# Kernel tuning notes

Measured on AMD Instinct MI355X. Metric: run time of the kernel, lower is better.

Reference implementation:

```python
import jax, jax.numpy as jnp
import numpy as np

EPS = 1e-7


def setup_inputs() -> dict:
    key = jax.random.key(0)
    k1, k2, k3 = jax.random.split(key, 3)
    B, IN, OUT = 256, 256, 512
    x = jax.random.uniform(k1, (B, IN), dtype=jnp.float32)
    w = jax.random.uniform(k2, (IN, OUT), dtype=jnp.float32)
    t = jax.random.uniform(k3, (B, OUT), dtype=jnp.float32)
    return {"x": x, "w": w, "t": t}


def reference(x, w, t):
    # x: [B, IN], w: [IN, OUT], t: [B, OUT]
    xe = x[:, :, None]          # [B, IN, 1]
    te = t[:, None, :]          # [B, 1, OUT]
    we = w[None, :, :]          # [1, IN, OUT]

    one = jnp.asarray(1.0, dtype=x.dtype)
    # rel_x: relevance of x, reduced over batch dim 0 -> [1, IN, OUT]
    rel_x = jnp.minimum(te / (xe + EPS), one).sum(axis=0, keepdims=True) \
            / xe.sum(axis=0, keepdims=True)
    # rel_w: relevance of w, reduced over IN dim -> [B, 1, OUT]
    rel_w = jnp.minimum(te / (we + EPS), one).sum(axis=-2, keepdims=True) \
            / xe.sum(axis=-2, keepdims=True)

    ind_x = jnp.argmax(xe * rel_x, axis=-2, keepdims=True)  # [B, 1, OUT]
    ind_w = jnp.argmax(rel_w * we, axis=-2, keepdims=True)  # [B, 1, OUT]

    inner_x = xe * jax.lax.stop_gradient(we)  # [B, IN, OUT]
    inner_w = jax.lax.stop_gradient(xe) * we  # [B, IN, OUT]

    chosen_x = jnp.take_along_axis(inner_x, ind_x, axis=-2).squeeze(-2)  # [B, OUT]
    chosen_w = jnp.take_along_axis(inner_w, ind_w, axis=-2).squeeze(-2)  # [B, OUT]
    return chosen_x, chosen_w
```

## Files before the change

kernel.cpp:

```cpp
#include <hip/hip_runtime.h>

constexpr int B   = 256;
constexpr int IN  = 256;
constexpr int OUT = 512;
constexpr double EPSD = 1e-7;

typedef unsigned long long ull;


__global__ __launch_bounds__(256) void k_setup(const float* __restrict__ x,
        double* __restrict__ rxd, double* __restrict__ part, float* __restrict__ xt) {
    const int tid = threadIdx.x;
    const int blk = blockIdx.x;
    if (blk < 32) {
        const int b0 = blk * 8;
        #pragma unroll
        for (int k = 0; k < 8; ++k)
            rxd[(b0 + k) * IN + tid] = 1.0 / ((double)x[(b0 + k) * IN + tid] + EPSD);
    } else if (blk < 40) {
        const int j = blk - 32, b0 = j * 32;
        double s0 = 0, s1 = 0, s2 = 0, s3 = 0;
        #pragma unroll
        for (int k = 0; k < 32; k += 4) {
            s0 += (double)x[(b0 + k + 0) * IN + tid];
            s1 += (double)x[(b0 + k + 1) * IN + tid];
            s2 += (double)x[(b0 + k + 2) * IN + tid];
            s3 += (double)x[(b0 + k + 3) * IN + tid];
        }
        part[j * IN + tid] = (s0 + s1) + (s2 + s3);
    } else {
        const int i0 = (blk - 40) * 32;
        for (int k = 0; k < 32; ++k)
            xt[(i0 + k) * B + tid] = x[tid * IN + (i0 + k)];
    }
}

__global__ __launch_bounds__(512, 2) void k_main(const float* __restrict__ w,
        const float* __restrict__ t, const double* __restrict__ rxd,
        const double* __restrict__ part, const float* __restrict__ xt,
        float* __restrict__ out) {
    const int tid  = threadIdx.x;
    const int half = tid >> 8;
    const int j    = tid & 255;
    const int o    = blockIdx.x * 2 + half;

    __shared__ double tc[2][B];
    __shared__ double rp[2][2][IN];
    __shared__ double rc[2][IN];
    __shared__ ull    keys[2][2][B];
    __shared__ ull    swv[8];

    {
        float wv = w[j * OUT + o];
        ull key = ((ull)__float_as_uint(wv) << 8) | (unsigned)(255 - j);
        #pragma unroll
        for (int off = 32; off; off >>= 1) {
            ull v = __shfl_down(key, off);
            key = v > key ? v : key;
        }
        if ((tid & 63) == 0) swv[tid >> 6] = key;
    }

    tc[half][j] = (double)t[j * OUT + o];
    double ps = 0.0;
    #pragma unroll
    for (int k = 0; k < 8; ++k) ps += part[k * IN + j];
    const double rcolv = 1.0 / ps;
    __syncthreads();

    ull wk = swv[half * 4];
    #pragma unroll
    for (int k = 1; k < 4; ++k) { ull v = swv[half * 4 + k]; wk = v > wk ? v : wk; }
    const int warg_o = 255 - (int)(wk & 0xFFull);

    {
        const int i0 = (j & 127) * 2;
        const int bh = j >> 7;
        const double* __restrict__ tcc  = tc[half] + bh * 128;
        const double* __restrict__ base = rxd + (size_t)(bh * 128) * IN + i0;
        double a0 = 0, a1 = 0, a2 = 0, a3 = 0;
        #pragma unroll 8
        for (int k = 0; k < 128; k += 2) {
            double2 r0 = *(const double2*)(base + (size_t)k * IN);
            double2 r1 = *(const double2*)(base + (size_t)(k + 1) * IN);
            double t0 = tcc[k], t1 = tcc[k + 1];
            a0 += fmin(t0 * r0.x, 1.0);
            a1 += fmin(t0 * r0.y, 1.0);
            a2 += fmin(t1 * r1.x, 1.0);
            a3 += fmin(t1 * r1.y, 1.0);
        }
        rp[half][bh][i0]     = a0 + a2;
        rp[half][bh][i0 + 1] = a1 + a3;
    }
    __syncthreads();
    rc[half][j] = (rp[half][0][j] + rp[half][1][j]) * rcolv;
    __syncthreads();

    {
        const int b0 = (j & 127) * 2;
        const int ih = j >> 7;
        const double* __restrict__ rcc = rc[half];
        double mA0 = -1.0, mA1 = -1.0, mB0 = -1.0, mB1 = -1.0;
        #pragma unroll 8
        for (int i = ih * 128; i < ih * 128 + 128; i += 2) {
            float2 x0 = *(const float2*)&xt[(size_t)i * B + b0];
            float2 x1 = *(const float2*)&xt[(size_t)(i + 1) * B + b0];
            double s00 = (double)x0.x * rcc[i];
            double s01 = (double)x0.y * rcc[i];
            double s10 = (double)x1.x * rcc[i + 1];
            double s11 = (double)x1.y * rcc[i + 1];
            long long u00 = (__double_as_longlong(s00) & ~0xFFll) | (long long)(255 - i);
            long long u01 = (__double_as_longlong(s01) & ~0xFFll) | (long long)(255 - i);
            long long u10 = (__double_as_longlong(s10) & ~0xFFll) | (long long)(255 - (i + 1));
            long long u11 = (__double_as_longlong(s11) & ~0xFFll) | (long long)(255 - (i + 1));
            mA0 = fmax(mA0, __longlong_as_double(u00));
            mB0 = fmax(mB0, __longlong_as_double(u01));
            mA1 = fmax(mA1, __longlong_as_double(u10));
            mB1 = fmax(mB1, __longlong_as_double(u11));
        }
        keys[half][ih][b0]     = (ull)__double_as_longlong(fmax(mA0, mA1));
        keys[half][ih][b0 + 1] = (ull)__double_as_longlong(fmax(mB0, mB1));
    }
    __syncthreads();

    {
        const int b = (j & 127) * 2 + (j >> 7);
        ull k0 = keys[half][0][b], k1 = keys[half][1][b];
        ull mk = k0 > k1 ? k0 : k1;
        const int ia = 255 - (int)(mk & 0xFFull);

        float* __restrict__ out0 = out;
        float* __restrict__ out1 = out + (size_t)B * OUT;
        out0[b * OUT + o] = xt[(size_t)ia * B + b] * w[ia * OUT + o];

        const int iw = (tc[half][b] > 0.0) ? warg_o : 0;
        out1[b * OUT + o] = xt[(size_t)iw * B + b] * w[iw * OUT + o];
    }
}

extern "C" void kernel_launch(void* const* d_in, const int* in_sizes, int n_in,
                              void* d_out, int out_size, void* d_ws, size_t ws_size,
                              hipStream_t stream) {
    const float* x = (const float*)d_in[0];
    const float* w = (const float*)d_in[1];
    const float* t = (const float*)d_in[2];
    float* out = (float*)d_out;

    double* dws  = (double*)d_ws;
    double* RXD  = dws;
    double* PART = RXD + (size_t)B * IN;
    float*  XT   = (float*)(PART + 8 * IN);

    k_setup<<<48, 256, 0, stream>>>(x, RXD, PART, XT);
    k_main<<<OUT / 2, 512, 0, stream>>>(w, t, RXD, PART, XT, out);
}
```

Baseline: 83.64 us.

## Split each output column across a full block and tile the transpose

The main kernel now launches one 512-thread block per output column instead of two columns per block. The batch and IN reductions are split four ways, with a final shared-memory combine, and the launch bound is raised to four blocks per CU. The setup transpose now uses a padded 64x64 shared tile so both reads and writes are coalesced, using 16 tiles instead of 8 strided blocks. The aim is to double grid parallelism and shorten per-thread loops, in exchange for half the threads idling in the serial phases and more blocks reading the rxd/xt tables.

```diff
diff --git a/kernel.cpp b/kernel.cpp
--- a/kernel.cpp
+++ b/kernel.cpp
@@ -29,28 +29,48 @@
         }
         part[j * IN + tid] = (s0 + s1) + (s2 + s3);
     } else {
-        const int i0 = (blk - 40) * 32;
-        for (int k = 0; k < 32; ++k)
-            xt[(i0 + k) * B + tid] = x[tid * IN + (i0 + k)];
+        __shared__ float tile[64][65];
+        const int tl  = blk - 40;
+        const int tr0 = (tl >> 2) * 64;
+        const int tc0 = (tl & 3) * 64;
+        const int c   = tid & 63;
+        const int r4  = tid >> 6;
+        #pragma unroll
+        for (int k = 0; k < 16; ++k) {
+            const int r = r4 + k * 4;
+            tile[r][c] = x[(tr0 + r) * IN + tc0 + c];
+        }
+        __syncthreads();
+        #pragma unroll
+        for (int k = 0; k < 16; ++k) {
+            const int r = r4 + k * 4;
+            xt[(size_t)(tc0 + r) * B + tr0 + c] = tile[c][r];
+        }
     }
 }
 
-__global__ __launch_bounds__(512, 2) void k_main(const float* __restrict__ w,
+__global__ __launch_bounds__(512, 4) void k_main(const float* __restrict__ w,
         const float* __restrict__ t, const double* __restrict__ rxd,
         const double* __restrict__ part, const float* __restrict__ xt,
         float* __restrict__ out) {
-    const int tid  = threadIdx.x;
-    const int half = tid >> 8;
-    const int j    = tid & 255;
-    const int o    = blockIdx.x * 2 + half;
+    const int tid = threadIdx.x;
+    const int j   = tid & 255;
+    const int o   = blockIdx.x;
 
-    __shared__ double tc[2][B];
-    __shared__ double rp[2][2][IN];
-    __shared__ double rc[2][IN];
-    __shared__ ull    keys[2][2][B];
-    __shared__ ull    swv[8];
+    __shared__ double tc[B];
+    __shared__ double rcs[IN];
+    __shared__ double rp[4][IN];
+    __shared__ double rc[IN];
+    __shared__ ull    keys[4][B];
+    __shared__ ull    swv[4];
 
-    {
+    int warg_o = 0;
+    if (tid < 256) {
+        tc[j] = (double)t[j * OUT + o];
+        double ps = 0.0;
+        #pragma unroll
+        for (int k = 0; k < 8; ++k) ps += part[k * IN + j];
+        rcs[j] = 1.0 / ps;
         float wv = w[j * OUT + o];
         ull key = ((ull)__float_as_uint(wv) << 8) | (unsigned)(255 - j);
         #pragma unroll
@@ -60,27 +80,22 @@
         }
         if ((tid & 63) == 0) swv[tid >> 6] = key;
     }
-
-    tc[half][j] = (double)t[j * OUT + o];
-    double ps = 0.0;
-    #pragma unroll
-    for (int k = 0; k < 8; ++k) ps += part[k * IN + j];
-    const double rcolv = 1.0 / ps;
     __syncthreads();
-
-    ull wk = swv[half * 4];
-    #pragma unroll
-    for (int k = 1; k < 4; ++k) { ull v = swv[half * 4 + k]; wk = v > wk ? v : wk; }
-    const int warg_o = 255 - (int)(wk & 0xFFull);
+    if (tid < 256) {
+        ull wk = swv[0];
+        #pragma unroll
+        for (int k = 1; k < 4; ++k) { ull v = swv[k]; wk = v > wk ? v : wk; }
+        warg_o = 255 - (int)(wk & 0xFFull);
+    }
 
     {
-        const int i0 = (j & 127) * 2;
-        const int bh = j >> 7;
-        const double* __restrict__ tcc  = tc[half] + bh * 128;
-        const double* __restrict__ base = rxd + (size_t)(bh * 128) * IN + i0;
+        const int i0 = (tid & 127) * 2;
+        const int bq = tid >> 7;
+        const double* __restrict__ tcc  = tc + bq * 64;
+        const double* __restrict__ base = rxd + (size_t)(bq * 64) * IN + i0;
         double a0 = 0, a1 = 0, a2 = 0, a3 = 0;
         #pragma unroll 8
-        for (int k = 0; k < 128; k += 2) {
+        for (int k = 0; k < 64; k += 2) {
             double2 r0 = *(const double2*)(base + (size_t)k * IN);
             double2 r1 = *(const double2*)(base + (size_t)(k + 1) * IN);
             double t0 = tcc[k], t1 = tcc[k + 1];
@@ -89,26 +104,26 @@
             a2 += fmin(t1 * r1.x, 1.0);
             a3 += fmin(t1 * r1.y, 1.0);
         }
-        rp[half][bh][i0]     = a0 + a2;
-        rp[half][bh][i0 + 1] = a1 + a3;
+        rp[bq][i0]     = a0 + a2;
+        rp[bq][i0 + 1] = a1 + a3;
     }
     __syncthreads();
-    rc[half][j] = (rp[half][0][j] + rp[half][1][j]) * rcolv;
+    if (tid < 256)
+        rc[j] = (((rp[0][j] + rp[1][j]) + (rp[2][j] + rp[3][j]))) * rcs[j];
     __syncthreads();
 
     {
-        const int b0 = (j & 127) * 2;
-        const int ih = j >> 7;
-        const double* __restrict__ rcc = rc[half];
+        const int b0 = (tid & 127) * 2;
+        const int iq = tid >> 7;
         double mA0 = -1.0, mA1 = -1.0, mB0 = -1.0, mB1 = -1.0;
         #pragma unroll 8
-        for (int i = ih * 128; i < ih * 128 + 128; i += 2) {
+        for (int i = iq * 64; i < iq * 64 + 64; i += 2) {
             float2 x0 = *(const float2*)&xt[(size_t)i * B + b0];
             float2 x1 = *(const float2*)&xt[(size_t)(i + 1) * B + b0];
-            double s00 = (double)x0.x * rcc[i];
-            double s01 = (double)x0.y * rcc[i];
-            double s10 = (double)x1.x * rcc[i + 1];
-            double s11 = (double)x1.y * rcc[i + 1];
+            double s00 = (double)x0.x * rc[i];
+            double s01 = (double)x0.y * rc[i];
+            double s10 = (double)x1.x * rc[i + 1];
+            double s11 = (double)x1.y * rc[i + 1];
             long long u00 = (__double_as_longlong(s00) & ~0xFFll) | (long long)(255 - i);
             long long u01 = (__double_as_longlong(s01) & ~0xFFll) | (long long)(255 - i);
             long long u10 = (__double_as_longlong(s10) & ~0xFFll) | (long long)(255 - (i + 1));
@@ -118,22 +133,23 @@
             mA1 = fmax(mA1, __longlong_as_double(u10));
             mB1 = fmax(mB1, __longlong_as_double(u11));
         }
-        keys[half][ih][b0]     = (ull)__double_as_longlong(fmax(mA0, mA1));
-        keys[half][ih][b0 + 1] = (ull)__double_as_longlong(fmax(mB0, mB1));
+        keys[iq][b0]     = (ull)__double_as_longlong(fmax(mA0, mA1));
+        keys[iq][b0 + 1] = (ull)__double_as_longlong(fmax(mB0, mB1));
     }
     __syncthreads();
 
-    {
-        const int b = (j & 127) * 2 + (j >> 7);
-        ull k0 = keys[half][0][b], k1 = keys[half][1][b];
-        ull mk = k0 > k1 ? k0 : k1;
+    if (tid < 256) {
+        const int b = j;
+        ull mk = keys[0][b];
+        #pragma unroll
+        for (int k = 1; k < 4; ++k) { ull v = keys[k][b]; mk = v > mk ? v : mk; }
         const int ia = 255 - (int)(mk & 0xFFull);
 
         float* __restrict__ out0 = out;
         float* __restrict__ out1 = out + (size_t)B * OUT;
         out0[b * OUT + o] = xt[(size_t)ia * B + b] * w[ia * OUT + o];
 
-        const int iw = (tc[half][b] > 0.0) ? warg_o : 0;
+        const int iw = (tc[b] > 0.0) ? warg_o : 0;
         out1[b * OUT + o] = xt[(size_t)iw * B + b] * w[iw * OUT + o];
     }
 }
@@ -151,6 +167,6 @@
     double* PART = RXD + (size_t)B * IN;
     float*  XT   = (float*)(PART + 8 * IN);
 
-    k_setup<<<48, 256, 0, stream>>>(x, RXD, PART, XT);
-    k_main<<<OUT / 2, 512, 0, stream>>>(w, t, RXD, PART, XT, out);
+    k_setup<<<56, 256, 0, stream>>>(x, RXD, PART, XT);
+    k_main<<<OUT, 512, 0, stream>>>(w, t, RXD, PART, XT, out);
 }
```

Measured after the change: 82.74 us, median of 2. Within noise of the previous version (-1.1%).

## Fuse setup and main kernels with a grid-wide atomic barrier

Applied to the files above, without the earlier changes.

Merges the preprocessing kernel into the main kernel. The first 152 blocks compute reciprocals, partial column sums and a shared-memory tiled transpose of x, then all 256 blocks wait at a global atomic-counter barrier before running the main relevance and argmax phase. The counter is zeroed with a memset before launch. This removes one kernel launch and its drain gap, and the transpose gets coalesced access. In exchange it adds a memset, a spin barrier that needs all 256 blocks to be resident at once (launch bounds raised to 4 blocks per SM), and larger shared memory.

```diff
diff --git a/kernel.cpp b/kernel.cpp
--- a/kernel.cpp
+++ b/kernel.cpp
@@ -7,50 +7,68 @@
 
 typedef unsigned long long ull;
 
-
-__global__ __launch_bounds__(256) void k_setup(const float* __restrict__ x,
-        double* __restrict__ rxd, double* __restrict__ part, float* __restrict__ xt) {
+__global__ __launch_bounds__(512, 4) void k_fused(
+        const float* __restrict__ x, const float* __restrict__ w,
+        const float* __restrict__ t,
+        double* __restrict__ rxd, double* __restrict__ part,
+        float* __restrict__ xt, unsigned* __restrict__ cnt,
+        float* __restrict__ out) {
     const int tid = threadIdx.x;
     const int blk = blockIdx.x;
-    if (blk < 32) {
-        const int b0 = blk * 8;
-        #pragma unroll
-        for (int k = 0; k < 8; ++k)
-            rxd[(b0 + k) * IN + tid] = 1.0 / ((double)x[(b0 + k) * IN + tid] + EPSD);
-    } else if (blk < 40) {
-        const int j = blk - 32, b0 = j * 32;
-        double s0 = 0, s1 = 0, s2 = 0, s3 = 0;
-        #pragma unroll
-        for (int k = 0; k < 32; k += 4) {
-            s0 += (double)x[(b0 + k + 0) * IN + tid];
-            s1 += (double)x[(b0 + k + 1) * IN + tid];
-            s2 += (double)x[(b0 + k + 2) * IN + tid];
-            s3 += (double)x[(b0 + k + 3) * IN + tid];
-        }
-        part[j * IN + tid] = (s0 + s1) + (s2 + s3);
-    } else {
-        const int i0 = (blk - 40) * 32;
-        for (int k = 0; k < 32; ++k)
-            xt[(i0 + k) * B + tid] = x[tid * IN + (i0 + k)];
-    }
-}
 
-__global__ __launch_bounds__(512, 2) void k_main(const float* __restrict__ w,
-        const float* __restrict__ t, const double* __restrict__ rxd,
-        const double* __restrict__ part, const float* __restrict__ xt,
-        float* __restrict__ out) {
-    const int tid  = threadIdx.x;
-    const int half = tid >> 8;
-    const int j    = tid & 255;
-    const int o    = blockIdx.x * 2 + half;
-
+    __shared__ float  tile[64][65];
+    __shared__ double sred[512];
     __shared__ double tc[2][B];
     __shared__ double rp[2][2][IN];
     __shared__ double rc[2][IN];
     __shared__ ull    keys[2][2][B];
     __shared__ ull    swv[8];
 
+    if (blk < 128) {
+        const int idx = blk * 512 + tid;
+        rxd[idx] = 1.0 / ((double)x[idx] + EPSD);
+    } else if (blk < 136) {
+        const int p = blk - 128;
+        const int i = tid & 255, h = tid >> 8;
+        const float* xr = x + (size_t)(p * 32 + h * 16) * IN + i;
+        double s0 = 0, s1 = 0;
+        #pragma unroll
+        for (int k = 0; k < 16; k += 2) {
+            s0 += (double)xr[k * IN];
+            s1 += (double)xr[(k + 1) * IN];
+        }
+        sred[tid] = s0 + s1;
+        __syncthreads();
+        if (h == 0) part[p * IN + i] = sred[i] + sred[256 + i];
+    } else if (blk < 152) {
+        const int tl = blk - 136;
+        const int r0 = (tl >> 2) * 64, c0 = (tl & 3) * 64;
+        const int c  = tid & 63, r8 = (tid >> 6) * 8;
+        #pragma unroll
+        for (int k = 0; k < 8; ++k)
+            tile[r8 + k][c] = x[(size_t)(r0 + r8 + k) * IN + c0 + c];
+        __syncthreads();
+        #pragma unroll
+        for (int k = 0; k < 8; ++k)
+            xt[(size_t)(c0 + r8 + k) * B + r0 + c] = tile[c][r8 + k];
+    }
+
+    __syncthreads();
+    if (tid == 0) {
+        __threadfence();
+        __hip_atomic_fetch_add(cnt, 1u, __ATOMIC_ACQ_REL, __HIP_MEMORY_SCOPE_AGENT);
+        while (__hip_atomic_load(cnt, __ATOMIC_ACQUIRE, __HIP_MEMORY_SCOPE_AGENT) < 256u)
+            __builtin_amdgcn_s_sleep(2);
+        __threadfence();
+    }
+    __syncthreads();
+
+    const int half = tid >> 8;
+    const int j    = tid & 255;
+    const int o    = blk * 2 + half;
+
     {
+        tc[half][j] = (double)t[j * OUT + o];
         float wv = w[j * OUT + o];
         ull key = ((ull)__float_as_uint(wv) << 8) | (unsigned)(255 - j);
         #pragma unroll
@@ -60,8 +78,6 @@
         }
         if ((tid & 63) == 0) swv[tid >> 6] = key;
     }
-
-    tc[half][j] = (double)t[j * OUT + o];
     double ps = 0.0;
     #pragma unroll
     for (int k = 0; k < 8; ++k) ps += part[k * IN + j];
@@ -124,7 +140,7 @@
     __syncthreads();
 
     {
-        const int b = (j & 127) * 2 + (j >> 7);
+        const int b = j;
         ull k0 = keys[half][0][b], k1 = keys[half][1][b];
         ull mk = k0 > k1 ? k0 : k1;
         const int ia = 255 - (int)(mk & 0xFFull);
@@ -146,11 +162,12 @@
     const float* t = (const float*)d_in[2];
     float* out = (float*)d_out;
 
-    double* dws  = (double*)d_ws;
-    double* RXD  = dws;
-    double* PART = RXD + (size_t)B * IN;
-    float*  XT   = (float*)(PART + 8 * IN);
+    double*   dws  = (double*)d_ws;
+    double*   RXD  = dws;
+    double*   PART = RXD + (size_t)B * IN;
+    float*    XT   = (float*)(PART + 8 * IN);
+    unsigned* CNT  = (unsigned*)(XT + (size_t)IN * B);
 
-    k_setup<<<48, 256, 0, stream>>>(x, RXD, PART, XT);
-    k_main<<<OUT / 2, 512, 0, stream>>>(w, t, RXD, PART, XT, out);
+    hipMemsetAsync(CNT, 0, sizeof(unsigned), stream);
+    k_fused<<<256, 512, 0, stream>>>(x, w, t, RXD, PART, XT, CNT, out);
 }
```

After: 111.2 us. +32.9%, slower.
